# Kernel optimization log

Hardware: AMD Instinct MI355X
Metric: run time of the kernel (lower is better)

Reference implementation:

```python
import jax, jax.numpy as jnp
import numpy as np

WINDOW_SIZES = (128, 256, 512)
EMBED_DIM = 512
B, T = 128, 65536


def _branch_tokens(signal, W, b, w):
    # Conv1d(in=1, out=E, kernel=w, stride=w, padding=0) == non-overlapping
    # patch projection: (B, S, w) @ (w, E) with S = T // w.
    Bsz, Tlen = signal.shape
    S = Tlen // w
    patches = signal[:, : S * w].reshape(Bsz, S, w)
    return jnp.einsum('bsw,ew->bse', patches, W) + b  # (B, S, E)


def setup_inputs() -> dict:
    key = jax.random.key(0)
    ks = jax.random.split(key, 9)
    signal = jax.random.normal(ks[0], (B, T), dtype=jnp.float32)
    signal_mask = jax.random.randint(ks[1], (B, T), 0, 2).astype(bool)
    branch_idx = jax.random.randint(ks[2], (B,), 0, len(WINDOW_SIZES), dtype=jnp.int32)
    params = {}
    for i, w in enumerate(WINDOW_SIZES):
        params[f'W{i}'] = jax.random.normal(ks[3 + 2 * i], (EMBED_DIM, w), dtype=jnp.float32) * 0.02
        params[f'b{i}'] = jax.random.normal(ks[4 + 2 * i], (EMBED_DIM,), dtype=jnp.float32) * 0.02
    return {'signal': signal, 'signal_mask': signal_mask, 'branch_idx': branch_idx, **params}


def reference(signal, signal_mask, branch_idx, W0, b0, W1, b1, W2, b2):
    Bsz, Tlen = signal.shape
    Ws = (W0, W1, W2)
    bs = (b0, b1, b2)
    branch_S = [Tlen // w for w in WINDOW_SIZES]
    S_max = max(branch_S)
    # Compute every branch for every sample (faithful to the original module).
    padded = []
    for w, Wi, bi, Si in zip(WINDOW_SIZES, Ws, bs, branch_S):
        t = _branch_tokens(signal, Wi, bi, w)  # (B, Si, E)
        padded.append(jnp.pad(t, ((0, 0), (0, S_max - Si), (0, 0))))
    stacked = jnp.stack(padded)  # (n_branches, B, S_max, E)
    gathered = stacked[branch_idx, jnp.arange(Bsz)]  # (B, S_max, E)

    lengths = signal_mask.astype(jnp.int32).sum(axis=1)  # (B,)
    w_arr = jnp.asarray(WINDOW_SIZES, dtype=jnp.int32)
    S_arr = jnp.asarray(branch_S, dtype=jnp.int32)
    n_valid = jnp.minimum(lengths // w_arr[branch_idx],
                          jnp.minimum(S_arr[branch_idx], S_max))  # (B,)
    padding_mask = jnp.arange(S_max, dtype=jnp.int32)[None, :] < n_valid[:, None]  # (B, S_max)
    tokens = jnp.where(padding_mask[..., None], gathered, jnp.zeros((), signal.dtype))
    return tokens, padding_mask
```

## Files before the change

### kernel.cpp

```cpp
#include <hip/hip_runtime.h>
#include <hip/hip_bf16.h>

#define BATCH 128
#define TLEN  65536
#define EDIM  512
#define SMAX  512

typedef __attribute__((ext_vector_type(8))) short   bf16x8;
typedef __attribute__((ext_vector_type(4))) float   floatx4;
typedef __attribute__((ext_vector_type(8))) ushort  ushort8;

__device__ __forceinline__ ushort f2bf(float f) {
  __hip_bfloat16 h = __float2bfloat16(f);
  return *reinterpret_cast<ushort*>(&h);
}

__device__ __forceinline__ void cvt16(ushort* dst, float4 a, float4 b,
                                      float4 c, float4 d) {
  ushort8 p0, p1;
  p0[0]=f2bf(a.x); p0[1]=f2bf(a.y); p0[2]=f2bf(a.z); p0[3]=f2bf(a.w);
  p0[4]=f2bf(b.x); p0[5]=f2bf(b.y); p0[6]=f2bf(b.z); p0[7]=f2bf(b.w);
  p1[0]=f2bf(c.x); p1[1]=f2bf(c.y); p1[2]=f2bf(c.z); p1[3]=f2bf(c.w);
  p1[4]=f2bf(d.x); p1[5]=f2bf(d.y); p1[6]=f2bf(d.z); p1[7]=f2bf(d.w);
  *(ushort8*)dst = p0; *(ushort8*)(dst + 8) = p1;
}

__device__ __forceinline__ void gl_lds16(const ushort* g, ushort* l) {
  __builtin_amdgcn_global_load_lds(
      (const __attribute__((address_space(1))) void*)g,
      (__attribute__((address_space(3))) void*)l, 16, 0, 0);
}

__global__ __launch_bounds__(256) void mask_partial_kernel(
    const int* __restrict__ mask, int* __restrict__ part) {
  const int b = blockIdx.x, c = blockIdx.y, t = threadIdx.x;
  const int4* row = (const int4*)(mask + (size_t)b * TLEN + (size_t)c * 8192);
  int s = 0;
  #pragma unroll
  for (int i = 0; i < 8; ++i) {
    int4 v = row[t + i * 256];
    s += (v.x != 0) + (v.y != 0) + (v.z != 0) + (v.w != 0);
  }
  #pragma unroll
  for (int off = 32; off > 0; off >>= 1) s += __shfl_down(s, off);
  __shared__ int partial[4];
  if ((t & 63) == 0) partial[t >> 6] = s;
  __syncthreads();
  if (t == 0)
    part[b * 8 + c] = partial[0] + partial[1] + partial[2] + partial[3];
}

__global__ __launch_bounds__(256) void mask_final_kernel(
    const int* __restrict__ part, const int* __restrict__ branch_idx,
    int* __restrict__ n_valid, float* __restrict__ out_mask) {
  const int b = blockIdx.x, t = threadIdx.x;
  __shared__ int nv_sh;
  if (t == 0) {
    int len = 0;
    #pragma unroll
    for (int i = 0; i < 8; ++i) len += part[b * 8 + i];
    int w = 128 << branch_idx[b];
    int nv = len / w;
    n_valid[b] = nv;
    nv_sh = nv;
  }
  __syncthreads();
  const int nv = nv_sh;
  out_mask[(size_t)b * SMAX + t]       = (t < nv)       ? 1.0f : 0.0f;
  out_mask[(size_t)b * SMAX + 256 + t] = (256 + t < nv) ? 1.0f : 0.0f;
}

#define SIGN  (BATCH * TLEN)
#define W0N   (EDIM * 128)
#define W1N   (EDIM * 256)
#define W2N   (EDIM * 512)
#define CVT_TOTAL (SIGN + W0N + W1N + W2N)

__global__ __launch_bounds__(256) void cvt_kernel(
    const float* __restrict__ sig, const float* __restrict__ W0,
    const float* __restrict__ W1, const float* __restrict__ W2,
    ushort* __restrict__ dst) {
  const size_t i = ((size_t)blockIdx.x * 256 + threadIdx.x) * 16;
  const float* src;
  if (i < SIGN)                  src = sig + i;
  else if (i < SIGN + W0N)       src = W0 + (i - SIGN);
  else if (i < SIGN + W0N + W1N) src = W1 + (i - SIGN - W0N);
  else                           src = W2 + (i - SIGN - W0N - W1N);
  const float4* s4 = (const float4*)src;
  cvt16(dst + i, s4[0], s4[1], s4[2], s4[3]);
}

template <int W>
__device__ __forceinline__ void gemm_mfma_body(
    const ushort* __restrict__ sigb, const ushort* __restrict__ Wp,
    const float* __restrict__ bp, float* __restrict__ outb,
    int nv, int s0, int e0, int t, ushort* Abuf, ushort* Bbuf) {
  constexpr int ITERS = W / 32;
  const int wave = t >> 6, lane = t & 63;
  const int lane16 = lane & 15, quad = lane >> 4;
  const int ws_ = (wave >> 1) * 64, we_ = (wave & 1) * 64;

  const int c0 = t,        r0 = c0 >> 2, kc0 = (c0 & 3) ^ (r0 & 3);
  const int c1 = t + 256,  r1 = c1 >> 2, kc1 = (c1 & 3) ^ (r1 & 3);
  const ushort* ag0 = sigb + (size_t)(s0 + r0) * W + kc0 * 8;
  const ushort* ag1 = sigb + (size_t)(s0 + r1) * W + kc1 * 8;
  const ushort* bg0 = Wp + (size_t)(e0 + r0) * W + kc0 * 8;
  const ushort* bg1 = Wp + (size_t)(e0 + r1) * W + kc1 * 8;
  ushort* al0 = Abuf + wave * 512;
  ushort* al1 = Abuf + 2048 + wave * 512;
  ushort* bl0 = Bbuf + wave * 512;
  ushort* bl1 = Bbuf + 2048 + wave * 512;

  floatx4 acc[4][4];
  #pragma unroll
  for (int i = 0; i < 4; ++i)
    #pragma unroll
    for (int j = 0; j < 4; ++j) acc[i][j] = (floatx4)(0.f);

  {
    gl_lds16(ag0, al0); gl_lds16(ag1, al1);
    gl_lds16(bg0, bl0); gl_lds16(bg1, bl1);
  }
  __syncthreads();

  const int slotq = (quad ^ (lane16 & 3)) * 8;

  #pragma unroll
  for (int k = 0; k < ITERS; ++k) {
    if (k + 1 < ITERS) {
      const size_t ko = (size_t)(k + 1) * 32;
      const int p = ((k + 1) & 1) * 4096;
      gl_lds16(ag0 + ko, al0 + p); gl_lds16(ag1 + ko, al1 + p);
      gl_lds16(bg0 + ko, bl0 + p); gl_lds16(bg1 + ko, bl1 + p);
    }
    const ushort* A = Abuf + (k & 1) * 4096;
    const ushort* B = Bbuf + (k & 1) * 4096;
    bf16x8 af[4], bfr[4];
    #pragma unroll
    for (int i = 0; i < 4; ++i)
      af[i] = *(const bf16x8*)&A[(ws_ + i * 16 + lane16) * 32 + slotq];
    #pragma unroll
    for (int j = 0; j < 4; ++j)
      bfr[j] = *(const bf16x8*)&B[(we_ + j * 16 + lane16) * 32 + slotq];
    #pragma unroll
    for (int i = 0; i < 4; ++i)
      #pragma unroll
      for (int j = 0; j < 4; ++j)
        acc[i][j] = __builtin_amdgcn_mfma_f32_16x16x32_bf16(af[i], bfr[j], acc[i][j], 0, 0, 0);
    __syncthreads();
  }

  float bval[4];
  #pragma unroll
  for (int j = 0; j < 4; ++j) bval[j] = bp[e0 + we_ + j * 16 + lane16];
  #pragma unroll
  for (int i = 0; i < 4; ++i) {
    #pragma unroll
    for (int rr = 0; rr < 4; ++rr) {
      const int s_row = s0 + ws_ + i * 16 + quad * 4 + rr;
      const bool valid = s_row < nv;
      float* op = outb + (size_t)s_row * EDIM + e0 + we_ + lane16;
      #pragma unroll
      for (int j = 0; j < 4; ++j)
        op[j * 16] = valid ? (acc[i][j][rr] + bval[j]) : 0.f;
    }
  }
}

__global__ __launch_bounds__(256) void gemm_bf_kernel(
    const ushort* __restrict__ sigbf, const int* __restrict__ branch_idx,
    const int* __restrict__ n_valid_arr,
    const ushort* __restrict__ W0b, const float* __restrict__ bias0,
    const ushort* __restrict__ W1b, const float* __restrict__ bias1,
    const ushort* __restrict__ W2b, const float* __restrict__ bias2,
    float* __restrict__ out) {
  const int et = blockIdx.x, st = blockIdx.y, b = blockIdx.z;
  const int t = threadIdx.x;
  const int s0 = st * 128, e0 = et * 128;
  const int bi = branch_idx[b];
  const int S_b = 512 >> bi;
  float* outb = out + (size_t)b * SMAX * EDIM;

  if (s0 >= S_b) {
    const float4 z = make_float4(0.f, 0.f, 0.f, 0.f);
    #pragma unroll
    for (int i = 0; i < 16; ++i) {
      int idx = t + i * 256;
      int r = idx >> 5, c = idx & 31;
      *(float4*)(outb + (size_t)(s0 + r) * EDIM + e0 + c * 4) = z;
    }
    return;
  }

  __shared__ __align__(16) ushort Abuf[2 * 4096];
  __shared__ __align__(16) ushort Bbuf[2 * 4096];
  const int nv = n_valid_arr[b];
  const ushort* sigb = sigbf + (size_t)b * TLEN;
  switch (bi) {
    case 0:  gemm_mfma_body<128>(sigb, W0b, bias0, outb, nv, s0, e0, t, Abuf, Bbuf); break;
    case 1:  gemm_mfma_body<256>(sigb, W1b, bias1, outb, nv, s0, e0, t, Abuf, Bbuf); break;
    default: gemm_mfma_body<512>(sigb, W2b, bias2, outb, nv, s0, e0, t, Abuf, Bbuf); break;
  }
}

#define LDS_STRIDE 40
#define BUFSZ (128 * LDS_STRIDE)

template <int W>
__device__ __forceinline__ void gemm_fb_body(
    const float* __restrict__ sigb, const float* __restrict__ Wp,
    const float* __restrict__ bp, float* __restrict__ outb,
    int nv, int s0, int e0, int t, ushort* Ab, ushort* Bb) {
  constexpr int ITERS = W / 32;
  const int wave = t >> 6, lane = t & 63;
  const int lane16 = lane & 15, quad = lane >> 4;
  const int ws_ = (wave >> 1) * 64, we_ = (wave & 1) * 64;
  const int r = t >> 1, h = t & 1;
  const float* asrc = sigb + (size_t)(s0 + r) * W + h * 16;
  const float* bsrc = Wp + (size_t)(e0 + r) * W + h * 16;
  {
    const float4* a4 = (const float4*)asrc;
    const float4* b4 = (const float4*)bsrc;
    cvt16(Ab + r * LDS_STRIDE + h * 16, a4[0], a4[1], a4[2], a4[3]);
    cvt16(Bb + r * LDS_STRIDE + h * 16, b4[0], b4[1], b4[2], b4[3]);
  }
  __syncthreads();
  floatx4 acc[4][4];
  #pragma unroll
  for (int i = 0; i < 4; ++i)
    #pragma unroll
    for (int j = 0; j < 4; ++j) acc[i][j] = (floatx4)(0.f);
  #pragma unroll
  for (int k = 0; k < ITERS; ++k) {
    const ushort* curA = Ab + (k & 1) * BUFSZ;
    const ushort* curB = Bb + (k & 1) * BUFSZ;
    float4 av0, av1, av2, av3, bv0, bv1, bv2, bv3;
    if (k + 1 < ITERS) {
      const float4* a4 = (const float4*)(asrc + (k + 1) * 32);
      const float4* b4 = (const float4*)(bsrc + (k + 1) * 32);
      av0 = a4[0]; av1 = a4[1]; av2 = a4[2]; av3 = a4[3];
      bv0 = b4[0]; bv1 = b4[1]; bv2 = b4[2]; bv3 = b4[3];
    }
    bf16x8 af[4], bfr[4];
    #pragma unroll
    for (int i = 0; i < 4; ++i)
      af[i] = *(const bf16x8*)&curA[(ws_ + i * 16 + lane16) * LDS_STRIDE + quad * 8];
    #pragma unroll
    for (int j = 0; j < 4; ++j)
      bfr[j] = *(const bf16x8*)&curB[(we_ + j * 16 + lane16) * LDS_STRIDE + quad * 8];
    #pragma unroll
    for (int i = 0; i < 4; ++i)
      #pragma unroll
      for (int j = 0; j < 4; ++j)
        acc[i][j] = __builtin_amdgcn_mfma_f32_16x16x32_bf16(af[i], bfr[j], acc[i][j], 0, 0, 0);
    if (k + 1 < ITERS) {
      cvt16(Ab + ((k + 1) & 1) * BUFSZ + r * LDS_STRIDE + h * 16, av0, av1, av2, av3);
      cvt16(Bb + ((k + 1) & 1) * BUFSZ + r * LDS_STRIDE + h * 16, bv0, bv1, bv2, bv3);
      __syncthreads();
    }
  }
  float bval[4];
  #pragma unroll
  for (int j = 0; j < 4; ++j) bval[j] = bp[e0 + we_ + j * 16 + lane16];
  #pragma unroll
  for (int i = 0; i < 4; ++i) {
    #pragma unroll
    for (int rr = 0; rr < 4; ++rr) {
      const int s_row = s0 + ws_ + i * 16 + quad * 4 + rr;
      const bool valid = s_row < nv;
      float* op = outb + (size_t)s_row * EDIM + e0 + we_ + lane16;
      #pragma unroll
      for (int j = 0; j < 4; ++j)
        op[j * 16] = valid ? (acc[i][j][rr] + bval[j]) : 0.f;
    }
  }
}

__global__ __launch_bounds__(256) void gemm_fb_kernel(
    const float* __restrict__ signal, const int* __restrict__ branch_idx,
    const int* __restrict__ n_valid_arr,
    const float* __restrict__ W0, const float* __restrict__ bias0,
    const float* __restrict__ W1, const float* __restrict__ bias1,
    const float* __restrict__ W2, const float* __restrict__ bias2,
    float* __restrict__ out) {
  const int et = blockIdx.x, st = blockIdx.y, b = blockIdx.z;
  const int t = threadIdx.x;
  const int s0 = st * 128, e0 = et * 128;
  const int bi = branch_idx[b];
  const int S_b = 512 >> bi;
  float* outb = out + (size_t)b * SMAX * EDIM;
  if (s0 >= S_b) {
    const float4 z = make_float4(0.f, 0.f, 0.f, 0.f);
    #pragma unroll
    for (int i = 0; i < 16; ++i) {
      int idx = t + i * 256;
      int r = idx >> 5, c = idx & 31;
      *(float4*)(outb + (size_t)(s0 + r) * EDIM + e0 + c * 4) = z;
    }
    return;
  }
  __shared__ __align__(16) ushort Ab[2 * BUFSZ];
  __shared__ __align__(16) ushort Bb[2 * BUFSZ];
  const int nv = n_valid_arr[b];
  const float* sigb = signal + (size_t)b * TLEN;
  switch (bi) {
    case 0:  gemm_fb_body<128>(sigb, W0, bias0, outb, nv, s0, e0, t, Ab, Bb); break;
    case 1:  gemm_fb_body<256>(sigb, W1, bias1, outb, nv, s0, e0, t, Ab, Bb); break;
    default: gemm_fb_body<512>(sigb, W2, bias2, outb, nv, s0, e0, t, Ab, Bb); break;
  }
}

extern "C" void kernel_launch(void* const* d_in, const int* in_sizes, int n_in,
                              void* d_out, int out_size, void* d_ws, size_t ws_size,
                              hipStream_t stream) {
  const float* signal = (const float*)d_in[0];
  const int*   mask   = (const int*)d_in[1];
  const int*   bidx   = (const int*)d_in[2];
  const float* W0 = (const float*)d_in[3];
  const float* b0 = (const float*)d_in[4];
  const float* W1 = (const float*)d_in[5];
  const float* b1 = (const float*)d_in[6];
  const float* W2 = (const float*)d_in[7];
  const float* b2 = (const float*)d_in[8];

  float* out_tokens = (float*)d_out;
  float* out_mask   = (float*)d_out + (size_t)BATCH * SMAX * EDIM;
  int*   n_valid    = (int*)d_ws;
  int*   part       = (int*)d_ws + 128;

  mask_partial_kernel<<<dim3(BATCH, 8), dim3(256), 0, stream>>>(mask, part);
  mask_final_kernel<<<dim3(BATCH), dim3(256), 0, stream>>>(part, bidx, n_valid, out_mask);

  const size_t need = 8192 + (size_t)CVT_TOTAL * 2;
  if (ws_size >= need) {
    ushort* cvt_base = (ushort*)((char*)d_ws + 8192);
    ushort* sig_bf = cvt_base;
    ushort* w0_bf  = cvt_base + SIGN;
    ushort* w1_bf  = w0_bf + W0N;
    ushort* w2_bf  = w1_bf + W1N;
    cvt_kernel<<<dim3(CVT_TOTAL / 4096), dim3(256), 0, stream>>>(
        signal, W0, W1, W2, cvt_base);
    gemm_bf_kernel<<<dim3(4, 4, BATCH), dim3(256), 0, stream>>>(
        sig_bf, bidx, n_valid, w0_bf, b0, w1_bf, b1, w2_bf, b2, out_tokens);
  } else {
    gemm_fb_kernel<<<dim3(4, 4, BATCH), dim3(256), 0, stream>>>(
        signal, bidx, n_valid, W0, b0, W1, b1, W2, b2, out_tokens);
  }
}
```

Before: 223.0 us.

## Fuse signal fp32-to-bf16 conversion into GEMM LDS fragment loads

Stops converting the whole 128x65536 signal to bf16 in a separate pass. The GEMM now streams fp32 signal tiles into LDS through direct global-to-LDS loads and converts them to bf16 while building MFMA fragments. Only the weights are still pre-converted. This removes a full read and write of the signal buffer, but doubles the A-tile LDS footprint and traffic and adds per-fragment conversion instructions to the inner loop.

```diff
diff --git a/kernel.cpp b/kernel.cpp
--- a/kernel.cpp
+++ b/kernel.cpp
@@ -25,7 +25,19 @@
   *(ushort8*)dst = p0; *(ushort8*)(dst + 8) = p1;
 }
 
-__device__ __forceinline__ void gl_lds16(const ushort* g, ushort* l) {
+__device__ __forceinline__ bf16x8 cvt_frag(float4 lo, float4 hi) {
+  ushort8 u;
+  u[0] = f2bf(lo.x); u[1] = f2bf(lo.y); u[2] = f2bf(lo.z); u[3] = f2bf(lo.w);
+  u[4] = f2bf(hi.x); u[5] = f2bf(hi.y); u[6] = f2bf(hi.z); u[7] = f2bf(hi.w);
+  return __builtin_bit_cast(bf16x8, u);
+}
+
+__device__ __forceinline__ void gl_lds16_f(const float* g, float* l) {
+  __builtin_amdgcn_global_load_lds(
+      (const __attribute__((address_space(1))) void*)g,
+      (__attribute__((address_space(3))) void*)l, 16, 0, 0);
+}
+__device__ __forceinline__ void gl_lds16_u(const ushort* g, ushort* l) {
   __builtin_amdgcn_global_load_lds(
       (const __attribute__((address_space(1))) void*)g,
       (__attribute__((address_space(3))) void*)l, 16, 0, 0);
@@ -70,46 +82,54 @@
   out_mask[(size_t)b * SMAX + 256 + t] = (256 + t < nv) ? 1.0f : 0.0f;
 }
 
-#define SIGN  (BATCH * TLEN)
 #define W0N   (EDIM * 128)
 #define W1N   (EDIM * 256)
 #define W2N   (EDIM * 512)
-#define CVT_TOTAL (SIGN + W0N + W1N + W2N)
-
-__global__ __launch_bounds__(256) void cvt_kernel(
-    const float* __restrict__ sig, const float* __restrict__ W0,
-    const float* __restrict__ W1, const float* __restrict__ W2,
-    ushort* __restrict__ dst) {
+#define WTOT  (W0N + W1N + W2N)
+
+__global__ __launch_bounds__(256) void cvtw_kernel(
+    const float* __restrict__ W0, const float* __restrict__ W1,
+    const float* __restrict__ W2, ushort* __restrict__ dst) {
   const size_t i = ((size_t)blockIdx.x * 256 + threadIdx.x) * 16;
   const float* src;
-  if (i < SIGN)                  src = sig + i;
-  else if (i < SIGN + W0N)       src = W0 + (i - SIGN);
-  else if (i < SIGN + W0N + W1N) src = W1 + (i - SIGN - W0N);
-  else                           src = W2 + (i - SIGN - W0N - W1N);
+  if (i < W0N)             src = W0 + i;
+  else if (i < W0N + W1N)  src = W1 + (i - W0N);
+  else                     src = W2 + (i - W0N - W1N);
   const float4* s4 = (const float4*)src;
   cvt16(dst + i, s4[0], s4[1], s4[2], s4[3]);
 }
 
 template <int W>
-__device__ __forceinline__ void gemm_mfma_body(
-    const ushort* __restrict__ sigb, const ushort* __restrict__ Wp,
+__device__ __forceinline__ void gemm_body(
+    const float* __restrict__ sigb, const ushort* __restrict__ Wp,
     const float* __restrict__ bp, float* __restrict__ outb,
-    int nv, int s0, int e0, int t, ushort* Abuf, ushort* Bbuf) {
+    int nv, int s0, int e0, int t, float* Af, ushort* Bu) {
   constexpr int ITERS = W / 32;
   const int wave = t >> 6, lane = t & 63;
   const int lane16 = lane & 15, quad = lane >> 4;
   const int ws_ = (wave >> 1) * 64, we_ = (wave & 1) * 64;
 
-  const int c0 = t,        r0 = c0 >> 2, kc0 = (c0 & 3) ^ (r0 & 3);
-  const int c1 = t + 256,  r1 = c1 >> 2, kc1 = (c1 & 3) ^ (r1 & 3);
-  const ushort* ag0 = sigb + (size_t)(s0 + r0) * W + kc0 * 8;
-  const ushort* ag1 = sigb + (size_t)(s0 + r1) * W + kc1 * 8;
-  const ushort* bg0 = Wp + (size_t)(e0 + r0) * W + kc0 * 8;
-  const ushort* bg1 = Wp + (size_t)(e0 + r1) * W + kc1 * 8;
-  ushort* al0 = Abuf + wave * 512;
-  ushort* al1 = Abuf + 2048 + wave * 512;
-  ushort* bl0 = Bbuf + wave * 512;
-  ushort* bl1 = Bbuf + 2048 + wave * 512;
+  const float* ag[4];
+  #pragma unroll
+  for (int i = 0; i < 4; ++i) {
+    const int c = t + i * 256;
+    const int row = c >> 3, kc = (c & 7) ^ (row & 7);
+    ag[i] = sigb + (size_t)(s0 + row) * W + kc * 4;
+  }
+  float* al[4];
+  #pragma unroll
+  for (int i = 0; i < 4; ++i) al[i] = Af + (i * 256 + wave * 64) * 4;
+
+  const ushort* bg[2];
+  #pragma unroll
+  for (int i = 0; i < 2; ++i) {
+    const int c = t + i * 256;
+    const int row = c >> 2, kc = (c & 3) ^ (row & 3);
+    bg[i] = Wp + (size_t)(e0 + row) * W + kc * 8;
+  }
+  ushort* bl[2];
+  #pragma unroll
+  for (int i = 0; i < 2; ++i) bl[i] = Bu + (i * 256 + wave * 64) * 8;
 
   floatx4 acc[4][4];
   #pragma unroll
@@ -117,31 +137,40 @@
     #pragma unroll
     for (int j = 0; j < 4; ++j) acc[i][j] = (floatx4)(0.f);
 
-  {
-    gl_lds16(ag0, al0); gl_lds16(ag1, al1);
-    gl_lds16(bg0, bl0); gl_lds16(bg1, bl1);
-  }
+  #pragma unroll
+  for (int i = 0; i < 4; ++i) gl_lds16_f(ag[i], al[i]);
+  #pragma unroll
+  for (int i = 0; i < 2; ++i) gl_lds16_u(bg[i], bl[i]);
   __syncthreads();
 
-  const int slotq = (quad ^ (lane16 & 3)) * 8;
+  const int pa0 = ((quad * 2) ^ (lane16 & 7)) * 4;
+  const int pa1 = ((quad * 2 + 1) ^ (lane16 & 7)) * 4;
+  const int pb  = (quad ^ (lane16 & 3)) * 8;
 
   #pragma unroll
   for (int k = 0; k < ITERS; ++k) {
     if (k + 1 < ITERS) {
-      const size_t ko = (size_t)(k + 1) * 32;
-      const int p = ((k + 1) & 1) * 4096;
-      gl_lds16(ag0 + ko, al0 + p); gl_lds16(ag1 + ko, al1 + p);
-      gl_lds16(bg0 + ko, bl0 + p); gl_lds16(bg1 + ko, bl1 + p);
-    }
-    const ushort* A = Abuf + (k & 1) * 4096;
-    const ushort* B = Bbuf + (k & 1) * 4096;
+      const int ko = (k + 1) * 32;
+      const int pa = ((k + 1) & 1) * 4096;
+      const int pbuf = ((k + 1) & 1) * 4096;
+      #pragma unroll
+      for (int i = 0; i < 4; ++i) gl_lds16_f(ag[i] + ko, al[i] + pa);
+      #pragma unroll
+      for (int i = 0; i < 2; ++i) gl_lds16_u(bg[i] + ko, bl[i] + pbuf);
+    }
+    const float* A = Af + (k & 1) * 4096;
+    const ushort* B = Bu + (k & 1) * 4096;
     bf16x8 af[4], bfr[4];
     #pragma unroll
-    for (int i = 0; i < 4; ++i)
-      af[i] = *(const bf16x8*)&A[(ws_ + i * 16 + lane16) * 32 + slotq];
+    for (int i = 0; i < 4; ++i) {
+      const int ra = ws_ + i * 16 + lane16;
+      float4 a0 = *(const float4*)(A + ra * 32 + pa0);
+      float4 a1 = *(const float4*)(A + ra * 32 + pa1);
+      af[i] = cvt_frag(a0, a1);
+    }
     #pragma unroll
     for (int j = 0; j < 4; ++j)
-      bfr[j] = *(const bf16x8*)&B[(we_ + j * 16 + lane16) * 32 + slotq];
+      bfr[j] = *(const bf16x8*)&B[(we_ + j * 16 + lane16) * 32 + pb];
     #pragma unroll
     for (int i = 0; i < 4; ++i)
       #pragma unroll
@@ -167,13 +196,11 @@
   }
 }
 
-__global__ __launch_bounds__(256) void gemm_bf_kernel(
-    const ushort* __restrict__ sigbf, const int* __restrict__ branch_idx,
-    const int* __restrict__ n_valid_arr,
-    const ushort* __restrict__ W0b, const float* __restrict__ bias0,
-    const ushort* __restrict__ W1b, const float* __restrict__ bias1,
-    const ushort* __restrict__ W2b, const float* __restrict__ bias2,
-    float* __restrict__ out) {
+__global__ __launch_bounds__(256) void gemm_kernel(
+    const float* __restrict__ signal, const int* __restrict__ branch_idx,
+    const int* __restrict__ n_valid_arr, const ushort* __restrict__ wbf,
+    const float* __restrict__ bias0, const float* __restrict__ bias1,
+    const float* __restrict__ bias2, float* __restrict__ out) {
   const int et = blockIdx.x, st = blockIdx.y, b = blockIdx.z;
   const int t = threadIdx.x;
   const int s0 = st * 128, e0 = et * 128;
@@ -192,14 +219,17 @@
     return;
   }
 
-  __shared__ __align__(16) ushort Abuf[2 * 4096];
-  __shared__ __align__(16) ushort Bbuf[2 * 4096];
+  __shared__ __align__(16) float  Af[2 * 4096];
+  __shared__ __align__(16) ushort Bu[2 * 4096];
   const int nv = n_valid_arr[b];
-  const ushort* sigb = sigbf + (size_t)b * TLEN;
+  const float* sigb = signal + (size_t)b * TLEN;
   switch (bi) {
-    case 0:  gemm_mfma_body<128>(sigb, W0b, bias0, outb, nv, s0, e0, t, Abuf, Bbuf); break;
-    case 1:  gemm_mfma_body<256>(sigb, W1b, bias1, outb, nv, s0, e0, t, Abuf, Bbuf); break;
-    default: gemm_mfma_body<512>(sigb, W2b, bias2, outb, nv, s0, e0, t, Abuf, Bbuf); break;
+    case 0:
+      gemm_body<128>(sigb, wbf, bias0, outb, nv, s0, e0, t, Af, Bu); break;
+    case 1:
+      gemm_body<256>(sigb, wbf + W0N, bias1, outb, nv, s0, e0, t, Af, Bu); break;
+    default:
+      gemm_body<512>(sigb, wbf + W0N + W1N, bias2, outb, nv, s0, e0, t, Af, Bu); break;
   }
 }
 
@@ -328,21 +358,17 @@
   int*   n_valid    = (int*)d_ws;
   int*   part       = (int*)d_ws + 128;
 
-  mask_partial_kernel<<<dim3(BATCH, 8), dim3(256), 0, stream>>>(mask, part);
-  mask_final_kernel<<<dim3(BATCH), dim3(256), 0, stream>>>(part, bidx, n_valid, out_mask);
-
-  const size_t need = 8192 + (size_t)CVT_TOTAL * 2;
+  const size_t need = 8192 + (size_t)WTOT * 2;
   if (ws_size >= need) {
-    ushort* cvt_base = (ushort*)((char*)d_ws + 8192);
-    ushort* sig_bf = cvt_base;
-    ushort* w0_bf  = cvt_base + SIGN;
-    ushort* w1_bf  = w0_bf + W0N;
-    ushort* w2_bf  = w1_bf + W1N;
-    cvt_kernel<<<dim3(CVT_TOTAL / 4096), dim3(256), 0, stream>>>(
-        signal, W0, W1, W2, cvt_base);
-    gemm_bf_kernel<<<dim3(4, 4, BATCH), dim3(256), 0, stream>>>(
-        sig_bf, bidx, n_valid, w0_bf, b0, w1_bf, b1, w2_bf, b2, out_tokens);
+    ushort* wbf = (ushort*)((char*)d_ws + 8192);
+    cvtw_kernel<<<dim3(WTOT / 4096), dim3(256), 0, stream>>>(W0, W1, W2, wbf);
+    mask_partial_kernel<<<dim3(BATCH, 8), dim3(256), 0, stream>>>(mask, part);
+    mask_final_kernel<<<dim3(BATCH), dim3(256), 0, stream>>>(part, bidx, n_valid, out_mask);
+    gemm_kernel<<<dim3(4, 4, BATCH), dim3(256), 0, stream>>>(
+        signal, bidx, n_valid, wbf, b0, b1, b2, out_tokens);
   } else {
+    mask_partial_kernel<<<dim3(BATCH, 8), dim3(256), 0, stream>>>(mask, part);
+    mask_final_kernel<<<dim3(BATCH), dim3(256), 0, stream>>>(part, bidx, n_valid, out_mask);
     gemm_fb_kernel<<<dim3(4, 4, BATCH), dim3(256), 0, stream>>>(
         signal, bidx, n_valid, W0, b0, W1, b1, W2, b2, out_tokens);
   }
```

After: 249.4 us. 11.8% more time.
